# Kernel optimization log

Measured on AMD Instinct MI355X. Metric: run time of the kernel, lower is better.

Reference implementation:

```python
import jax, jax.numpy as jnp
import numpy as np

EPS_LOG = 1e-8
EPS_CHECK = 1e-4


def to_float8(x, exp_bits=4, mant_bits=3):
    # fp8 emulation: sign/abs/log2/floor/clamp/round chain
    max_exp = 2 ** (exp_bits - 1) - 1
    min_exp = -max_exp
    scale = 2.0 ** mant_bits
    sign = jnp.sign(x)
    x_abs = jnp.abs(x)
    exp = jnp.clip(jnp.floor(jnp.log2(x_abs + EPS_LOG)), min_exp, max_exp)
    pow2 = jnp.exp2(exp)
    mant = x_abs / pow2 - 1.0
    mant_q = jnp.round(mant * scale) / scale
    return sign * (1.0 + mant_q) * pow2


def checksum_verify(left, right, epsilon=EPS_CHECK):
    # ABFT: augment left with a column-sum row, right with a row-sum column
    left_cs = jnp.concatenate([left, jnp.sum(left, axis=0, keepdims=True)], axis=0)
    right_cs = jnp.concatenate([right, jnp.sum(right, axis=1, keepdims=True)], axis=1)
    prod_cs = left_cs @ right_cs  # [(m+1), (n+1)]
    output = prod_cs[:-1, :-1]
    row_sum_check = prod_cs[:-1, -1]
    col_sum_check = prod_cs[-1, :-1]
    col_diff = jnp.abs(jnp.sum(output, axis=0) - col_sum_check)
    row_diff = jnp.abs(jnp.sum(output, axis=1) - row_sum_check)
    mask = (row_diff > epsilon)[:, None] & (col_diff > epsilon)[None, :]
    return output, mask


def setup_inputs() -> dict:
    key = jax.random.key(0)
    kx, ku, kA, kB, kC = jax.random.split(key, 5)
    batch, n, m, p = 4096, 2048, 1024, 1024
    return {
        "x": jax.random.normal(kx, (batch, n), dtype=jnp.float32),
        "u": jax.random.normal(ku, (batch, m), dtype=jnp.float32),
        "A": jax.random.normal(kA, (n, n), dtype=jnp.float32),
        "B": jax.random.normal(kB, (n, m), dtype=jnp.float32),
        "C": jax.random.normal(kC, (p, n), dtype=jnp.float32),
    }


def reference(x, u, A, B, C):
    int_bits, frac_bits = 4, 3
    Aq = to_float8(A, int_bits, frac_bits)
    Bq = to_float8(B, int_bits, frac_bits)
    left_term, left_mask = checksum_verify(x, Aq.T)
    right_term, right_mask = checksum_verify(u, Bq.T)
    x_next = to_float8(left_term + right_term, int_bits, frac_bits)
    _ = left_mask | right_mask  # mask computed but discarded in forward (as in torch)
    Cq = to_float8(C, int_bits, frac_bits)
    y = to_float8(x_next @ Cq.T, int_bits, frac_bits)
    return (x_next, y)
```

## Files before the change

kernel.cpp:

```cpp
#include <hip/hip_runtime.h>
#include <hip/hip_bf16.h>
#include <stdint.h>

typedef __bf16 bf16_t;
typedef __attribute__((ext_vector_type(8))) __bf16 bf16x8;
typedef __attribute__((ext_vector_type(4))) __bf16 bf16x4;
typedef __attribute__((ext_vector_type(4))) float f32x4;

__device__ __forceinline__ float q8(float v) {
    float a = __builtin_fabsf(v);
    float z = a + 1e-8f;
    int ei = ((__float_as_int(z) >> 23) & 0xff) - 127;
    ei = ei > 7 ? 7 : (ei < -7 ? -7 : ei);
    float p  = __int_as_float((ei + 127) << 23);
    float ip = __int_as_float((127 - ei) << 23);
    float m  = __builtin_fmaf(a, ip, -1.0f);
    float mq = __builtin_rintf(m * 8.0f) * 0.125f;
    float r  = (1.0f + mq) * p;
    return v < 0.0f ? -r : r;
}

__device__ __forceinline__ void gload_lds16(const bf16_t* g, bf16_t* l) {
    __builtin_amdgcn_global_load_lds(
        (__attribute__((address_space(1))) void*)(g),
        (__attribute__((address_space(3))) void*)(l), 16, 0, 0);
}

__global__ void pack_all(const float* __restrict__ x, const float* __restrict__ u,
                         const float* __restrict__ A, const float* __restrict__ B,
                         const float* __restrict__ C,
                         bf16_t* __restrict__ XU, bf16_t* __restrict__ AB,
                         bf16_t* __restrict__ CQ) {
    unsigned bid = blockIdx.x;
    if (bid < 12288u) {
        unsigned row = bid / 3u, piece = bid - row * 3u;
        int col = (piece * 256 + threadIdx.x) * 4;
        float4 v;
        if (col < 2048) v = *(const float4*)&x[(size_t)row * 2048 + col];
        else            v = *(const float4*)&u[(size_t)row * 1024 + (col - 2048)];
        bf16x4 o = { (bf16_t)v.x, (bf16_t)v.y, (bf16_t)v.z, (bf16_t)v.w };
        *(bf16x4*)&XU[(size_t)row * 3072 + col] = o;
    } else if (bid < 18432u) {
        unsigned b = bid - 12288u;
        unsigned row = b / 3u, piece = b - row * 3u;
        int col = (piece * 256 + threadIdx.x) * 4;
        float4 v;
        if (col < 2048) v = *(const float4*)&A[(size_t)row * 2048 + col];
        else            v = *(const float4*)&B[(size_t)row * 1024 + (col - 2048)];
        bf16x4 o = { (bf16_t)q8(v.x), (bf16_t)q8(v.y), (bf16_t)q8(v.z), (bf16_t)q8(v.w) };
        *(bf16x4*)&AB[(size_t)row * 3072 + col] = o;
    } else {
        unsigned b = bid - 18432u;
        unsigned row = b >> 1, piece = b & 1u;
        int col = (piece * 256 + threadIdx.x) * 4;
        float4 v = *(const float4*)&C[(size_t)row * 2048 + col];
        bf16x4 o = { (bf16_t)q8(v.x), (bf16_t)q8(v.y), (bf16_t)q8(v.z), (bf16_t)q8(v.w) };
        *(bf16x4*)&CQ[(size_t)row * 2048 + col] = o;
    }
}

template<int BN, bool DUAL>
__global__ __launch_bounds__(512, 4)
void gemm_q8_kernel(const bf16_t* __restrict__ A, const bf16_t* __restrict__ B,
                    float* __restrict__ outf, bf16_t* __restrict__ outb,
                    int M, int N, int K) {
    constexpr int BM = 128;
    constexpr int BK = 128;
    constexpr int NI = BN / 32;
    constexpr int A_ITS = BM * (BK / 8) / 512;
    constexpr int B_ITS = BN * (BK / 8) / 512;

    __shared__ alignas(16) bf16_t sA[BM * BK];
    __shared__ alignas(16) bf16_t sB[BN * BK];

    const int tid  = threadIdx.x;
    const int lane = tid & 63;
    const int wave = tid >> 6;
    const int wm   = wave & 3;
    const int wn   = wave >> 2;
    const int ln16 = lane & 15;
    const int quad = lane >> 4;

    const int brow = blockIdx.y * BM;
    const int bcol = blockIdx.x * BN;

    const bf16_t* gA[A_ITS]; bf16_t* lA[A_ITS];
#pragma unroll
    for (int it = 0; it < A_ITS; ++it) {
        int L = it * 512 + tid;
        int r = L >> 4, c = L & 15;
        gA[it] = A + (size_t)(brow + r) * K + (c ^ (r & 15)) * 8;
        lA[it] = sA + (it * 512 + wave * 64) * 8;
    }
    const bf16_t* gB[B_ITS]; bf16_t* lB[B_ITS];
#pragma unroll
    for (int it = 0; it < B_ITS; ++it) {
        int L = it * 512 + tid;
        int r = L >> 4, c = L & 15;
        gB[it] = B + (size_t)(bcol + r) * K + (c ^ (r & 15)) * 8;
        lB[it] = sB + (it * 512 + wave * 64) * 8;
    }

    int a_off[2][4], b_off[NI][4];
#pragma unroll
    for (int im = 0; im < 2; ++im) {
        int r = wm * 32 + im * 16 + ln16;
#pragma unroll
        for (int s = 0; s < 4; ++s) {
            int cg = s * 4 + quad;
            a_off[im][s] = (r * 16 + (cg ^ (r & 15))) * 8;
        }
    }
#pragma unroll
    for (int in = 0; in < NI; ++in) {
        int r = wn * (BN / 2) + in * 16 + ln16;
#pragma unroll
        for (int s = 0; s < 4; ++s) {
            int cg = s * 4 + quad;
            b_off[in][s] = (r * 16 + (cg ^ (r & 15))) * 8;
        }
    }

    f32x4 acc[2][NI];
#pragma unroll
    for (int im = 0; im < 2; ++im)
#pragma unroll
        for (int in = 0; in < NI; ++in)
            acc[im][in] = (f32x4){0.f, 0.f, 0.f, 0.f};

    for (int kt = 0; kt < K; kt += BK) {
#pragma unroll
        for (int it = 0; it < A_ITS; ++it) gload_lds16(gA[it], lA[it]);
#pragma unroll
        for (int it = 0; it < B_ITS; ++it) gload_lds16(gB[it], lB[it]);
#pragma unroll
        for (int it = 0; it < A_ITS; ++it) gA[it] += BK;
#pragma unroll
        for (int it = 0; it < B_ITS; ++it) gB[it] += BK;
        __syncthreads();
#pragma unroll
        for (int s = 0; s < 4; ++s) {
            bf16x8 af[2], bfv[NI];
#pragma unroll
            for (int im = 0; im < 2; ++im) af[im]  = *(const bf16x8*)(sA + a_off[im][s]);
#pragma unroll
            for (int in = 0; in < NI; ++in) bfv[in] = *(const bf16x8*)(sB + b_off[in][s]);
#pragma unroll
            for (int im = 0; im < 2; ++im)
#pragma unroll
                for (int in = 0; in < NI; ++in)
                    acc[im][in] = __builtin_amdgcn_mfma_f32_16x16x32_bf16(
                        af[im], bfv[in], acc[im][in], 0, 0, 0);
        }
        __syncthreads();
    }

    const int rbase = quad * 4;
#pragma unroll
    for (int im = 0; im < 2; ++im) {
#pragma unroll
        for (int in = 0; in < NI; ++in) {
            int gm = brow + wm * 32 + im * 16 + rbase;
            int gn = bcol + wn * (BN / 2) + in * 16 + ln16;
#pragma unroll
            for (int r = 0; r < 4; ++r) {
                float v = q8(acc[im][in][r]);
                outf[(size_t)(gm + r) * N + gn] = v;
                if (DUAL) outb[(size_t)(gm + r) * N + gn] = (bf16_t)v;
            }
        }
    }
}

extern "C" void kernel_launch(void* const* d_in, const int* in_sizes, int n_in,
                              void* d_out, int out_size, void* d_ws, size_t ws_size,
                              hipStream_t stream) {
    const float* x = (const float*)d_in[0];
    const float* u = (const float*)d_in[1];
    const float* A = (const float*)d_in[2];
    const float* B = (const float*)d_in[3];
    const float* C = (const float*)d_in[4];

    float* outf = (float*)d_out;
    float* xnf  = outf;
    float* yf   = outf + (size_t)4096 * 2048;

    uint8_t* ws = (uint8_t*)d_ws;
    bf16_t* XU = (bf16_t*)ws;
    bf16_t* AB = (bf16_t*)(ws + (size_t)25165824);
    bf16_t* CQ = (bf16_t*)(ws + (size_t)25165824 + 12582912);
    bf16_t* XN = (bf16_t*)(ws + (size_t)25165824 + 12582912 + 4194304);

    pack_all<<<dim3(20480), 256, 0, stream>>>(x, u, A, B, C, XU, AB, CQ);

    gemm_q8_kernel<128, true><<<dim3(2048 / 128, 4096 / 128), 512, 0, stream>>>(
        XU, AB, xnf, XN, 4096, 2048, 3072);
    gemm_q8_kernel<64, false><<<dim3(1024 / 64, 4096 / 128), 512, 0, stream>>>(
        XN, CQ, yf, nullptr, 4096, 1024, 2048);
}
```

Baseline: 203.3 us.

## Rewrite GEMM with 32x32 MFMA, double-buffered LDS and 256-thread blocks

Replaces the 16x16x32 MFMA GEMM with a 256-thread, 128x128 tile kernel using 32x32x16 bf16 MFMA, where each wave computes a 64x64 sub-tile. The K-step drops to 64 and the loop double-buffers shared memory, so the next tile loads while the current one is computed. The aim is more MFMA work per LDS read and hiding global-load latency. In exchange each block has fewer threads, the second GEMM launches only 8x32 blocks so the grid is smaller, and accumulator register pressure goes up.

```diff
diff --git a/kernel.cpp b/kernel.cpp
--- a/kernel.cpp
+++ b/kernel.cpp
@@ -5,7 +5,7 @@
 typedef __bf16 bf16_t;
 typedef __attribute__((ext_vector_type(8))) __bf16 bf16x8;
 typedef __attribute__((ext_vector_type(4))) __bf16 bf16x4;
-typedef __attribute__((ext_vector_type(4))) float f32x4;
+typedef __attribute__((ext_vector_type(16))) float f32x16;
 
 __device__ __forceinline__ float q8(float v) {
     float a = __builtin_fabsf(v);
@@ -59,114 +59,117 @@
     }
 }
 
-template<int BN, bool DUAL>
-__global__ __launch_bounds__(512, 4)
-void gemm_q8_kernel(const bf16_t* __restrict__ A, const bf16_t* __restrict__ B,
-                    float* __restrict__ outf, bf16_t* __restrict__ outb,
-                    int M, int N, int K) {
-    constexpr int BM = 128;
-    constexpr int BK = 128;
-    constexpr int NI = BN / 32;
-    constexpr int A_ITS = BM * (BK / 8) / 512;
-    constexpr int B_ITS = BN * (BK / 8) / 512;
-
-    __shared__ alignas(16) bf16_t sA[BM * BK];
-    __shared__ alignas(16) bf16_t sB[BN * BK];
+template<bool DUAL>
+__global__ __launch_bounds__(256, 2)
+void gemm32_q8(const bf16_t* __restrict__ A, const bf16_t* __restrict__ B,
+               float* __restrict__ outf, bf16_t* __restrict__ outb,
+               int M, int N, int K) {
+    constexpr int BM = 128, BN = 128, BK = 64;
+    constexpr int TILE = BM * BK;
+
+    __shared__ alignas(16) bf16_t sA[2][TILE];
+    __shared__ alignas(16) bf16_t sB[2][TILE];
 
     const int tid  = threadIdx.x;
     const int lane = tid & 63;
     const int wave = tid >> 6;
-    const int wm   = wave & 3;
-    const int wn   = wave >> 2;
-    const int ln16 = lane & 15;
-    const int quad = lane >> 4;
+    const int wm   = wave & 1;
+    const int wn   = wave >> 1;
+    const int ln32 = lane & 31;
+    const int hi   = lane >> 5;
 
     const int brow = blockIdx.y * BM;
     const int bcol = blockIdx.x * BN;
 
-    const bf16_t* gA[A_ITS]; bf16_t* lA[A_ITS];
-#pragma unroll
-    for (int it = 0; it < A_ITS; ++it) {
-        int L = it * 512 + tid;
-        int r = L >> 4, c = L & 15;
-        gA[it] = A + (size_t)(brow + r) * K + (c ^ (r & 15)) * 8;
-        lA[it] = sA + (it * 512 + wave * 64) * 8;
-    }
-    const bf16_t* gB[B_ITS]; bf16_t* lB[B_ITS];
-#pragma unroll
-    for (int it = 0; it < B_ITS; ++it) {
-        int L = it * 512 + tid;
-        int r = L >> 4, c = L & 15;
-        gB[it] = B + (size_t)(bcol + r) * K + (c ^ (r & 15)) * 8;
-        lB[it] = sB + (it * 512 + wave * 64) * 8;
-    }
-
-    int a_off[2][4], b_off[NI][4];
+    const bf16_t* gA[4]; const bf16_t* gB[4];
+#pragma unroll
+    for (int it = 0; it < 4; ++it) {
+        int r = it * 32 + (tid >> 3);
+        int c = (tid & 7) ^ (r & 7);
+        gA[it] = A + (size_t)(brow + r) * K + c * 8;
+        gB[it] = B + (size_t)(bcol + r) * K + c * 8;
+    }
+
+    auto stage = [&](int b) {
+#pragma unroll
+        for (int it = 0; it < 4; ++it) {
+            gload_lds16(gA[it], &sA[b][(it * 256 + wave * 64) * 8]);
+            gA[it] += BK;
+        }
+#pragma unroll
+        for (int it = 0; it < 4; ++it) {
+            gload_lds16(gB[it], &sB[b][(it * 256 + wave * 64) * 8]);
+            gB[it] += BK;
+        }
+    };
+
+    int a_off[2][4], b_off[2][4];
 #pragma unroll
     for (int im = 0; im < 2; ++im) {
-        int r = wm * 32 + im * 16 + ln16;
+        int r = wm * 64 + im * 32 + ln32;
 #pragma unroll
         for (int s = 0; s < 4; ++s) {
-            int cg = s * 4 + quad;
-            a_off[im][s] = (r * 16 + (cg ^ (r & 15))) * 8;
-        }
-    }
-#pragma unroll
-    for (int in = 0; in < NI; ++in) {
-        int r = wn * (BN / 2) + in * 16 + ln16;
+            int cg = s * 2 + hi;
+            a_off[im][s] = (r * 8 + (cg ^ (r & 7))) * 8;
+        }
+    }
+#pragma unroll
+    for (int in = 0; in < 2; ++in) {
+        int r = wn * 64 + in * 32 + ln32;
 #pragma unroll
         for (int s = 0; s < 4; ++s) {
-            int cg = s * 4 + quad;
-            b_off[in][s] = (r * 16 + (cg ^ (r & 15))) * 8;
-        }
-    }
-
-    f32x4 acc[2][NI];
+            int cg = s * 2 + hi;
+            b_off[in][s] = (r * 8 + (cg ^ (r & 7))) * 8;
+        }
+    }
+
+    f32x16 acc[2][2];
 #pragma unroll
     for (int im = 0; im < 2; ++im)
 #pragma unroll
-        for (int in = 0; in < NI; ++in)
-            acc[im][in] = (f32x4){0.f, 0.f, 0.f, 0.f};
-
-    for (int kt = 0; kt < K; kt += BK) {
-#pragma unroll
-        for (int it = 0; it < A_ITS; ++it) gload_lds16(gA[it], lA[it]);
-#pragma unroll
-        for (int it = 0; it < B_ITS; ++it) gload_lds16(gB[it], lB[it]);
-#pragma unroll
-        for (int it = 0; it < A_ITS; ++it) gA[it] += BK;
-#pragma unroll
-        for (int it = 0; it < B_ITS; ++it) gB[it] += BK;
+        for (int in = 0; in < 2; ++in)
+            acc[im][in] = (f32x16)(0.0f);
+
+    auto compute = [&](int b) {
+#pragma unroll
+        for (int s = 0; s < 4; ++s) {
+            bf16x8 af[2], bfv[2];
+#pragma unroll
+            for (int im = 0; im < 2; ++im) af[im]  = *(const bf16x8*)(&sA[b][a_off[im][s]]);
+#pragma unroll
+            for (int in = 0; in < 2; ++in) bfv[in] = *(const bf16x8*)(&sB[b][b_off[in][s]]);
+#pragma unroll
+            for (int im = 0; im < 2; ++im)
+#pragma unroll
+                for (int in = 0; in < 2; ++in)
+                    acc[im][in] = __builtin_amdgcn_mfma_f32_32x32x16_bf16(
+                        af[im], bfv[in], acc[im][in], 0, 0, 0);
+        }
+    };
+
+    const int T = K / BK;
+    stage(0);
+    for (int t = 0; t < T; t += 2) {
         __syncthreads();
-#pragma unroll
-        for (int s = 0; s < 4; ++s) {
-            bf16x8 af[2], bfv[NI];
-#pragma unroll
-            for (int im = 0; im < 2; ++im) af[im]  = *(const bf16x8*)(sA + a_off[im][s]);
-#pragma unroll
-            for (int in = 0; in < NI; ++in) bfv[in] = *(const bf16x8*)(sB + b_off[in][s]);
-#pragma unroll
-            for (int im = 0; im < 2; ++im)
-#pragma unroll
-                for (int in = 0; in < NI; ++in)
-                    acc[im][in] = __builtin_amdgcn_mfma_f32_16x16x32_bf16(
-                        af[im], bfv[in], acc[im][in], 0, 0, 0);
-        }
+        stage(1);
+        compute(0);
         __syncthreads();
-    }
-
-    const int rbase = quad * 4;
+        if (t + 2 < T) stage(0);
+        compute(1);
+    }
+
 #pragma unroll
     for (int im = 0; im < 2; ++im) {
 #pragma unroll
-        for (int in = 0; in < NI; ++in) {
-            int gm = brow + wm * 32 + im * 16 + rbase;
-            int gn = bcol + wn * (BN / 2) + in * 16 + ln16;
-#pragma unroll
-            for (int r = 0; r < 4; ++r) {
-                float v = q8(acc[im][in][r]);
-                outf[(size_t)(gm + r) * N + gn] = v;
-                if (DUAL) outb[(size_t)(gm + r) * N + gn] = (bf16_t)v;
+        for (int in = 0; in < 2; ++in) {
+            int gn = bcol + wn * 64 + in * 32 + ln32;
+#pragma unroll
+            for (int reg = 0; reg < 16; ++reg) {
+                int row = (reg & 3) + 8 * (reg >> 2) + 4 * hi;
+                int gm = brow + wm * 64 + im * 32 + row;
+                float v = q8(acc[im][in][reg]);
+                outf[(size_t)gm * N + gn] = v;
+                if (DUAL) outb[(size_t)gm * N + gn] = (bf16_t)v;
             }
         }
     }
@@ -193,8 +196,8 @@
 
     pack_all<<<dim3(20480), 256, 0, stream>>>(x, u, A, B, C, XU, AB, CQ);
 
-    gemm_q8_kernel<128, true><<<dim3(2048 / 128, 4096 / 128), 512, 0, stream>>>(
+    gemm32_q8<true><<<dim3(2048 / 128, 4096 / 128), 256, 0, stream>>>(
         XU, AB, xnf, XN, 4096, 2048, 3072);
-    gemm_q8_kernel<64, false><<<dim3(1024 / 64, 4096 / 128), 512, 0, stream>>>(
+    gemm32_q8<false><<<dim3(1024 / 128, 4096 / 128), 256, 0, stream>>>(
         XN, CQ, yf, nullptr, 4096, 1024, 2048);
 }
```

New measurement: 230.8 us. 1.14x slower.

## Double-buffer LDS tiles with BK=64 to overlap global loads and MFMA

Applied to the files above, without the earlier changes.

Halves the K tile from 128 to 64 and splits shared memory into two ping-pong buffers of the same total size. The next K-slice is issued via global_load_lds into the idle buffer before the MFMA work on the current one, so load latency can hide behind compute. The XOR swizzle and fragment offsets are rewritten for 8-chunk rows. The cost is twice as many barriers per K step and shorter compute phases between them. The code also assumes the number of K tiles is even, which holds for both GEMMs here.

```diff
diff --git a/kernel.cpp b/kernel.cpp
--- a/kernel.cpp
+++ b/kernel.cpp
@@ -65,13 +65,13 @@
                     float* __restrict__ outf, bf16_t* __restrict__ outb,
                     int M, int N, int K) {
     constexpr int BM = 128;
-    constexpr int BK = 128;
+    constexpr int BK = 64;
     constexpr int NI = BN / 32;
     constexpr int A_ITS = BM * (BK / 8) / 512;
     constexpr int B_ITS = BN * (BK / 8) / 512;
 
-    __shared__ alignas(16) bf16_t sA[BM * BK];
-    __shared__ alignas(16) bf16_t sB[BN * BK];
+    __shared__ alignas(16) bf16_t sA[2][BM * BK];
+    __shared__ alignas(16) bf16_t sB[2][BN * BK];
 
     const int tid  = threadIdx.x;
     const int lane = tid & 63;
@@ -84,40 +84,51 @@
     const int brow = blockIdx.y * BM;
     const int bcol = blockIdx.x * BN;
 
-    const bf16_t* gA[A_ITS]; bf16_t* lA[A_ITS];
+    const bf16_t* gA[A_ITS];
 #pragma unroll
     for (int it = 0; it < A_ITS; ++it) {
         int L = it * 512 + tid;
-        int r = L >> 4, c = L & 15;
-        gA[it] = A + (size_t)(brow + r) * K + (c ^ (r & 15)) * 8;
-        lA[it] = sA + (it * 512 + wave * 64) * 8;
-    }
-    const bf16_t* gB[B_ITS]; bf16_t* lB[B_ITS];
+        int r = L >> 3, c = L & 7;
+        gA[it] = A + (size_t)(brow + r) * K + (c ^ (r & 7)) * 8;
+    }
+    const bf16_t* gB[B_ITS];
 #pragma unroll
     for (int it = 0; it < B_ITS; ++it) {
         int L = it * 512 + tid;
-        int r = L >> 4, c = L & 15;
-        gB[it] = B + (size_t)(bcol + r) * K + (c ^ (r & 15)) * 8;
-        lB[it] = sB + (it * 512 + wave * 64) * 8;
-    }
-
-    int a_off[2][4], b_off[NI][4];
+        int r = L >> 3, c = L & 7;
+        gB[it] = B + (size_t)(bcol + r) * K + (c ^ (r & 7)) * 8;
+    }
+
+    auto stage = [&](int b) {
+#pragma unroll
+        for (int it = 0; it < A_ITS; ++it) {
+            gload_lds16(gA[it], &sA[b][(it * 512 + wave * 64) * 8]);
+            gA[it] += BK;
+        }
+#pragma unroll
+        for (int it = 0; it < B_ITS; ++it) {
+            gload_lds16(gB[it], &sB[b][(it * 512 + wave * 64) * 8]);
+            gB[it] += BK;
+        }
+    };
+
+    int a_off[2][2], b_off[NI][2];
 #pragma unroll
     for (int im = 0; im < 2; ++im) {
         int r = wm * 32 + im * 16 + ln16;
 #pragma unroll
-        for (int s = 0; s < 4; ++s) {
+        for (int s = 0; s < 2; ++s) {
             int cg = s * 4 + quad;
-            a_off[im][s] = (r * 16 + (cg ^ (r & 15))) * 8;
+            a_off[im][s] = (r * 8 + (cg ^ (r & 7))) * 8;
         }
     }
 #pragma unroll
     for (int in = 0; in < NI; ++in) {
         int r = wn * (BN / 2) + in * 16 + ln16;
 #pragma unroll
-        for (int s = 0; s < 4; ++s) {
+        for (int s = 0; s < 2; ++s) {
             int cg = s * 4 + quad;
-            b_off[in][s] = (r * 16 + (cg ^ (r & 15))) * 8;
+            b_off[in][s] = (r * 8 + (cg ^ (r & 7))) * 8;
         }
     }
 
@@ -128,23 +139,14 @@
         for (int in = 0; in < NI; ++in)
             acc[im][in] = (f32x4){0.f, 0.f, 0.f, 0.f};
 
-    for (int kt = 0; kt < K; kt += BK) {
-#pragma unroll
-        for (int it = 0; it < A_ITS; ++it) gload_lds16(gA[it], lA[it]);
-#pragma unroll
-        for (int it = 0; it < B_ITS; ++it) gload_lds16(gB[it], lB[it]);
-#pragma unroll
-        for (int it = 0; it < A_ITS; ++it) gA[it] += BK;
-#pragma unroll
-        for (int it = 0; it < B_ITS; ++it) gB[it] += BK;
-        __syncthreads();
-#pragma unroll
-        for (int s = 0; s < 4; ++s) {
+    auto compute = [&](int b) {
+#pragma unroll
+        for (int s = 0; s < 2; ++s) {
             bf16x8 af[2], bfv[NI];
 #pragma unroll
-            for (int im = 0; im < 2; ++im) af[im]  = *(const bf16x8*)(sA + a_off[im][s]);
-#pragma unroll
-            for (int in = 0; in < NI; ++in) bfv[in] = *(const bf16x8*)(sB + b_off[in][s]);
+            for (int im = 0; im < 2; ++im) af[im]  = *(const bf16x8*)(&sA[b][a_off[im][s]]);
+#pragma unroll
+            for (int in = 0; in < NI; ++in) bfv[in] = *(const bf16x8*)(&sB[b][b_off[in][s]]);
 #pragma unroll
             for (int im = 0; im < 2; ++im)
 #pragma unroll
@@ -152,7 +154,17 @@
                     acc[im][in] = __builtin_amdgcn_mfma_f32_16x16x32_bf16(
                         af[im], bfv[in], acc[im][in], 0, 0, 0);
         }
+    };
+
+    const int T = K / BK;
+    stage(0);
+    for (int t = 0; t < T; t += 2) {
         __syncthreads();
+        stage(1);
+        compute(0);
+        __syncthreads();
+        if (t + 2 < T) stage(0);
+        compute(1);
     }
 
     const int rbase = quad * 4;
```

New measurement: 210.4 us. 3.5% more time.
